# Kernel tuning notes

Hardware: AMD Instinct MI355X
Metric: run time of the kernel (lower is better)

The kernel has to match this reference:

```python
import jax, jax.numpy as jnp
import numpy as np

D_MODEL = 1024
N_HEADS = 16
HEAD_DIM = D_MODEL // N_HEADS  # 64
BASE = 10000.0
MAX_X, MAX_Y, MAX_Z = 32, 32, 8
NEG_INF = -1e9  # stand-in for float('-inf') in masked_fill; identical after softmax


def _split_dims(head_dim):
    n_pairs = head_dim // 2
    px = n_pairs // 3
    py = n_pairs // 3
    pz = n_pairs - px - py
    return px * 2, py * 2, pz * 2


def _cos_sin_table(dim, max_pos):
    # matches RotaryEmbedding3D._register_cache
    inv_freq = 1.0 / (BASE ** (np.arange(0, dim, 2, dtype=np.float32) / dim))
    t = np.arange(max_pos, dtype=np.float32)[:, None] * inv_freq  # [max_pos, dim/2]
    cos = np.repeat(np.cos(t), 2, axis=-1)  # repeat_interleave(2)
    sin = np.repeat(np.sin(t), 2, axis=-1)
    return jnp.asarray(cos), jnp.asarray(sin)


def _rotate_half(x):
    x1 = x[..., ::2]
    x2 = x[..., 1::2]
    return jnp.stack((-x2, x1), axis=-1).reshape(x.shape)


def setup_inputs() -> dict:
    key = jax.random.key(0)
    k1, k2, k3, k4, k5, k6 = jax.random.split(key, 6)
    B, S = 2, 2048
    hidden_states = jax.random.normal(k1, (B, S, D_MODEL), dtype=jnp.float32)
    w_qkv = jax.random.normal(k2, (D_MODEL, 3 * D_MODEL), dtype=jnp.float32) * 0.02
    w_out = jax.random.normal(k3, (D_MODEL, D_MODEL), dtype=jnp.float32) * 0.02
    px = jax.random.randint(k4, (B, S, 1), 0, MAX_X)
    py = jax.random.randint(k5, (B, S, 1), 0, MAX_Y)
    pz = jax.random.randint(k6, (B, S, 1), 0, MAX_Z)
    pos_xyz = jnp.concatenate([px, py, pz], axis=-1).astype(jnp.int64)
    causal_mask = jnp.triu(jnp.ones((S, S), dtype=bool), k=1)[None, None]  # [1,1,S,S]
    return {"hidden_states": hidden_states, "w_qkv": w_qkv, "w_out": w_out,
            "pos_xyz": pos_xyz, "causal_mask": causal_mask}


def reference(hidden_states, w_qkv, w_out, pos_xyz, causal_mask):
    B, S, D = hidden_states.shape
    H, Hd = N_HEADS, HEAD_DIM
    # fused QKV projection
    qkv = hidden_states @ w_qkv  # [B,S,3D]
    qkv = qkv.reshape(B, S, 3, H, Hd).transpose(2, 0, 3, 1, 4)  # [3,B,H,S,Hd]
    q, k, v = qkv[0], qkv[1], qkv[2]
    # 3D RoPE tables and lookups
    dx, dy, dz = _split_dims(Hd)
    cx, sx = _cos_sin_table(dx, MAX_X)
    cy, sy = _cos_sin_table(dy, MAX_Y)
    cz, sz = _cos_sin_table(dz, MAX_Z)
    ix = jnp.clip(pos_xyz[..., 0], 0, MAX_X - 1)
    iy = jnp.clip(pos_xyz[..., 1], 0, MAX_Y - 1)
    iz = jnp.clip(pos_xyz[..., 2], 0, MAX_Z - 1)
    cos = jnp.concatenate([cx[ix], cy[iy], cz[iz]], axis=-1)[:, None]  # [B,1,S,Hd]
    sin = jnp.concatenate([sx[ix], sy[iy], sz[iz]], axis=-1)[:, None]
    q = q * cos + _rotate_half(q) * sin
    k = k * cos + _rotate_half(k) * sin
    # SDPA with causal bias
    scale = Hd ** -0.5
    scores = jnp.einsum('bhqd,bhkd->bhqk', q, k) * scale
    scores = jnp.where(causal_mask, jnp.asarray(NEG_INF, scores.dtype), scores)
    probs = jax.nn.softmax(scores, axis=-1)
    attn = jnp.einsum('bhqk,bhkd->bhqd', probs, v)
    attn = attn.transpose(0, 2, 1, 3).reshape(B, S, D)
    return attn @ w_out
```

## Files before the change

kernel.cpp:

```cpp
#include <hip/hip_runtime.h>
#include <hip/hip_bf16.h>
#include <math.h>

typedef __bf16 bf16;
typedef __bf16 bf16x8 __attribute__((ext_vector_type(8)));
typedef float f32x4 __attribute__((ext_vector_type(4)));

#define SEQ 2048
#define NHEADS 16
#define HDIM 64
#define DM 1024
#define NEGBIG -1.0e30f

__device__ __forceinline__ void gload_lds16(const void* g, void* l) {
  __builtin_amdgcn_global_load_lds(
      (const __attribute__((address_space(1))) unsigned int*)g,
      (__attribute__((address_space(3))) unsigned int*)l, 16, 0, 0);
}

template <int CTRL>
__device__ __forceinline__ float dppmovf(float x) {
  return __builtin_bit_cast(
      float, __builtin_amdgcn_mov_dpp(__builtin_bit_cast(int, x), CTRL, 0xf,
                                      0xf, true));
}
__device__ __forceinline__ float rowmax16(float x) {
  x = fmaxf(x, dppmovf<0xB1>(x));
  x = fmaxf(x, dppmovf<0x4E>(x));
  x = fmaxf(x, dppmovf<0x124>(x));
  x = fmaxf(x, dppmovf<0x128>(x));
  return x;
}
__device__ __forceinline__ float rowsum16(float x) {
  x += dppmovf<0xB1>(x);
  x += dppmovf<0x4E>(x);
  x += dppmovf<0x124>(x);
  x += dppmovf<0x128>(x);
  return x;
}

__global__ __launch_bounds__(256) void cvt_f32_bf16(
    const float* __restrict__ in, bf16* __restrict__ out) {
  int i = (blockIdx.x * 256 + threadIdx.x) * 8;
  float4 a = *(const float4*)(in + i);
  float4 b = *(const float4*)(in + i + 4);
  bf16x8 o;
  o[0] = (bf16)a.x; o[1] = (bf16)a.y; o[2] = (bf16)a.z; o[3] = (bf16)a.w;
  o[4] = (bf16)b.x; o[5] = (bf16)b.y; o[6] = (bf16)b.z; o[7] = (bf16)b.w;
  *(bf16x8*)(out + i) = o;
}

__global__ __launch_bounds__(256) void transpose_f32_bf16(
    const float* __restrict__ in, bf16* __restrict__ out, int R, int C) {
  __shared__ float tile[64][65];
  int t = threadIdx.x;
  int c0 = blockIdx.x * 64, r0 = blockIdx.y * 64;
  int col = t & 63, rb = (t >> 6) * 16;
#pragma unroll
  for (int i = 0; i < 16; ++i)
    tile[rb + i][col] = in[(size_t)(r0 + rb + i) * C + c0 + col];
  __syncthreads();
#pragma unroll
  for (int i = 0; i < 16; ++i)
    out[(size_t)(c0 + rb + i) * R + r0 + col] = (bf16)tile[col][rb + i];
}

template <int EPI>
__global__ __launch_bounds__(256) void gemm_bt(
    const bf16* __restrict__ A, const bf16* __restrict__ Bt,
    float* __restrict__ C, int M, int N, int K,
    bf16* __restrict__ q_ws, bf16* __restrict__ k_ws, bf16* __restrict__ vT_ws,
    const int* __restrict__ pos) {
  __shared__ __align__(16) bf16 a_lds[128 * 32];
  __shared__ __align__(16) bf16 b_lds[128 * 32];
  int tid = threadIdx.x;
  int wave = tid >> 6, lane = tid & 63;
  int quad = lane >> 4, l15 = lane & 15;
  int wm = wave >> 1, wn = wave & 1;
  int m0 = blockIdx.y * 128, n0 = blockIdx.x * 128;

  f32x4 acc[4][4] = {};

  for (int kt = 0; kt < K; kt += 32) {
    __syncthreads();
#pragma unroll
    for (int call = 0; call < 2; ++call) {
      int chunk = call * 256 + tid;
      int row = chunk >> 2, cc = (chunk & 3) * 8;
      gload_lds16(A + (size_t)(m0 + row) * K + kt + cc,
                  (char*)a_lds + call * 4096 + wave * 1024);
      gload_lds16(Bt + (size_t)(n0 + row) * K + kt + cc,
                  (char*)b_lds + call * 4096 + wave * 1024);
    }
    __syncthreads();
    bf16x8 af[4], bfr[4];
#pragma unroll
    for (int i = 0; i < 4; ++i) {
      af[i]  = *(const bf16x8*)(a_lds + (wm * 64 + i * 16 + l15) * 32 + quad * 8);
      bfr[i] = *(const bf16x8*)(b_lds + (wn * 64 + i * 16 + l15) * 32 + quad * 8);
    }
#pragma unroll
    for (int mi = 0; mi < 4; ++mi)
#pragma unroll
      for (int ni = 0; ni < 4; ++ni)
        acc[mi][ni] = __builtin_amdgcn_mfma_f32_16x16x32_bf16(
            af[mi], bfr[ni], acc[mi][ni], 0, 0, 0);
  }

  if (EPI == 0) {
#pragma unroll
    for (int mi = 0; mi < 4; ++mi) {
      int mb = m0 + wm * 64 + mi * 16 + quad * 4;
#pragma unroll
      for (int ni = 0; ni < 4; ++ni) {
        int n = n0 + wn * 64 + ni * 16 + l15;
#pragma unroll
        for (int r = 0; r < 4; ++r)
          C[(size_t)(mb + r) * N + n] = acc[mi][ni][r];
      }
    }
  } else {
    const float LN1E4 = 9.210340371976184f;
#pragma unroll
    for (int mi = 0; mi < 4; ++mi) {
#pragma unroll
      for (int r = 0; r < 4; ++r) {
        int m = m0 + wm * 64 + mi * 16 + quad * 4 + r;
        int b = m >> 11, s = m & 2047;
        int px = pos[m * 3 + 0], py = pos[m * 3 + 1], pz = pos[m * 3 + 2];
        px = px < 0 ? 0 : (px > 31 ? 31 : px);
        py = py < 0 ? 0 : (py > 31 ? 31 : py);
        pz = pz < 0 ? 0 : (pz > 7 ? 7 : pz);
#pragma unroll
        for (int ni = 0; ni < 4; ++ni) {
          int n = n0 + wn * 64 + ni * 16 + l15;
          float v = acc[mi][ni][r];
          float partner = __shfl_xor(v, 1, 64);
          int which = n >> 10, nn = n & 1023, h = nn >> 6, hd = nn & 63;
          if (which == 2) {
            vT_ws[((size_t)(b * NHEADS + h) * HDIM + hd) * SEQ + s] = (bf16)v;
          } else {
            int i = hd >> 1, p, d, iloc;
            if (hd < 20)      { p = px; d = 20; iloc = i; }
            else if (hd < 40) { p = py; d = 20; iloc = i - 10; }
            else              { p = pz; d = 24; iloc = i - 20; }
            float invf = __expf(-((float)(2 * iloc) / (float)d) * LN1E4);
            float ang = (float)p * invf;
            float sn, cs;
            __sincosf(ang, &sn, &cs);
            float outv =
                (hd & 1) ? (v * cs + partner * sn) : (v * cs - partner * sn);
            bf16* dst = (which == 0) ? q_ws : k_ws;
            dst[((size_t)(b * NHEADS + h) * SEQ + s) * HDIM + hd] = (bf16)outv;
          }
        }
      }
    }
  }
}

__global__ __launch_bounds__(256) void attn_fwd(
    const bf16* __restrict__ Q, const bf16* __restrict__ K,
    const bf16* __restrict__ VT, bf16* __restrict__ O) {
  __shared__ __align__(16) bf16 k_lds[64 * 72];
  __shared__ __align__(16) bf16 v_lds[64 * 72];
  __shared__ __align__(16) bf16 p_lds[64 * 72];
  int tid = threadIdx.x;
  int wave = tid >> 6, lane = tid & 63;
  int quad = lane >> 4, l15 = lane & 15;
  int idx = blockIdx.x;
  int bh = idx & 31;
  int qt = 31 - (idx >> 5);
  int q0 = qt * 64;
  size_t base = (size_t)bh * SEQ * HDIM;
  const bf16* Qb = Q + base;
  const bf16* Kb = K + base;
  const bf16* VTb = VT + base;
  bf16* pw = p_lds + wave * 16 * 72;

  bf16x8 qf0 = *(const bf16x8*)(Qb + (size_t)(q0 + wave * 16 + l15) * HDIM + quad * 8);
  bf16x8 qf1 = *(const bf16x8*)(Qb + (size_t)(q0 + wave * 16 + l15) * HDIM + 32 + quad * 8);

  int c0 = tid * 2;
  int srow = c0 >> 3;
  int soff = (c0 & 7) * 8;

  f32x4 o_acc[4] = {};
  float m_i[4], l_i[4];
#pragma unroll
  for (int r = 0; r < 4; ++r) { m_i[r] = NEGBIG; l_i[r] = 0.f; }
  int qrow[4];
#pragma unroll
  for (int r = 0; r < 4; ++r) qrow[r] = q0 + wave * 16 + quad * 4 + r;

  for (int tkv = 0; tkv <= qt; ++tkv) {
    int kv0 = tkv * 64;
    __syncthreads();
    {
      const bf16* ksrc = Kb + (size_t)(kv0 + srow) * HDIM + soff;
      const bf16* vsrc = VTb + (size_t)srow * SEQ + kv0 + soff;
      bf16x8 ka = *(const bf16x8*)ksrc, kb2 = *(const bf16x8*)(ksrc + 8);
      bf16x8 va = *(const bf16x8*)vsrc, vb2 = *(const bf16x8*)(vsrc + 8);
      *(bf16x8*)(k_lds + srow * 72 + soff) = ka;
      *(bf16x8*)(k_lds + srow * 72 + soff + 8) = kb2;
      *(bf16x8*)(v_lds + srow * 72 + soff) = va;
      *(bf16x8*)(v_lds + srow * 72 + soff + 8) = vb2;
    }
    __syncthreads();
    f32x4 s_acc[4];
#pragma unroll
    for (int nt = 0; nt < 4; ++nt) {
      const bf16* krow_p = k_lds + (nt * 16 + l15) * 72;
      bf16x8 kf0 = *(const bf16x8*)(krow_p + quad * 8);
      bf16x8 kf1 = *(const bf16x8*)(krow_p + 32 + quad * 8);
      f32x4 z = {};
      z = __builtin_amdgcn_mfma_f32_16x16x32_bf16(qf0, kf0, z, 0, 0, 0);
      z = __builtin_amdgcn_mfma_f32_16x16x32_bf16(qf1, kf1, z, 0, 0, 0);
      s_acc[nt] = z;
    }
    bool diag = (tkv == qt);
#pragma unroll
    for (int r = 0; r < 4; ++r) {
      float mx = NEGBIG;
#pragma unroll
      for (int nt = 0; nt < 4; ++nt) {
        float v = fminf(s_acc[nt][r] * 0.125f, 3.0e38f);
        if (diag && (kv0 + nt * 16 + l15 > qrow[r])) v = NEGBIG;
        s_acc[nt][r] = v;
        mx = fmaxf(mx, v);
      }
      mx = rowmax16(mx);
      float mnew = fmaxf(m_i[r], mx);
      float alpha = __expf(m_i[r] - mnew);
      float rs = 0.f;
#pragma unroll
      for (int nt = 0; nt < 4; ++nt) {
        float p = __expf(s_acc[nt][r] - mnew);
        s_acc[nt][r] = p;
        rs += p;
      }
      rs = rowsum16(rs);
      l_i[r] = l_i[r] * alpha + rs;
      m_i[r] = mnew;
#pragma unroll
      for (int nt = 0; nt < 4; ++nt) o_acc[nt][r] *= alpha;
#pragma unroll
      for (int nt = 0; nt < 4; ++nt)
        pw[(quad * 4 + r) * 72 + nt * 16 + l15] = (bf16)s_acc[nt][r];
    }
    __asm__ volatile("s_waitcnt lgkmcnt(0)" ::: "memory");
    bf16x8 pf0 = *(const bf16x8*)(pw + l15 * 72 + quad * 8);
    bf16x8 pf1 = *(const bf16x8*)(pw + l15 * 72 + 32 + quad * 8);
#pragma unroll
    for (int nt = 0; nt < 4; ++nt) {
      const bf16* vrow = v_lds + (nt * 16 + l15) * 72;
      bf16x8 vf0 = *(const bf16x8*)(vrow + quad * 8);
      bf16x8 vf1 = *(const bf16x8*)(vrow + 32 + quad * 8);
      o_acc[nt] = __builtin_amdgcn_mfma_f32_16x16x32_bf16(pf0, vf0, o_acc[nt], 0, 0, 0);
      o_acc[nt] = __builtin_amdgcn_mfma_f32_16x16x32_bf16(pf1, vf1, o_acc[nt], 0, 0, 0);
    }
  }
  int b = bh >> 4, h = bh & 15;
#pragma unroll
  for (int r = 0; r < 4; ++r) {
    float inv = 1.f / l_i[r];
    int s = q0 + wave * 16 + quad * 4 + r;
#pragma unroll
    for (int nt = 0; nt < 4; ++nt) {
      int d = nt * 16 + l15;
      O[((size_t)(b * SEQ + s)) * DM + h * HDIM + d] = (bf16)(o_acc[nt][r] * inv);
    }
  }
}

extern "C" void kernel_launch(void* const* d_in, const int* in_sizes, int n_in,
                              void* d_out, int out_size, void* d_ws,
                              size_t ws_size, hipStream_t stream) {
  const float* hidden = (const float*)d_in[0];
  const float* w_qkv  = (const float*)d_in[1];
  const float* w_out  = (const float*)d_in[2];
  const int*   pos    = (const int*)d_in[3];
  float* out = (float*)d_out;

  char* ws = (char*)d_ws;
  bf16* wqkvT  = (bf16*)ws;  ws += (size_t)3072 * 1024 * 2;
  bf16* woutT  = (bf16*)ws;  ws += (size_t)1024 * 1024 * 2;
  bf16* hid_bf = (bf16*)ws;  ws += (size_t)4096 * 1024 * 2;
  bf16* q_ws   = (bf16*)ws;  ws += (size_t)32 * SEQ * HDIM * 2;
  bf16* k_ws   = (bf16*)ws;  ws += (size_t)32 * SEQ * HDIM * 2;
  bf16* vT_ws  = (bf16*)ws;  ws += (size_t)32 * SEQ * HDIM * 2;
  bf16* attn_ws = (bf16*)ws;

  cvt_f32_bf16<<<dim3(2048), 256, 0, stream>>>(hidden, hid_bf);
  transpose_f32_bf16<<<dim3(48, 16), 256, 0, stream>>>(w_qkv, wqkvT, 1024, 3072);
  transpose_f32_bf16<<<dim3(16, 16), 256, 0, stream>>>(w_out, woutT, 1024, 1024);
  gemm_bt<1><<<dim3(24, 32), 256, 0, stream>>>(
      hid_bf, wqkvT, nullptr, 4096, 3072, 1024, q_ws, k_ws, vT_ws, pos);
  attn_fwd<<<dim3(1024), 256, 0, stream>>>(q_ws, k_ws, vT_ws, attn_ws);
  gemm_bt<0><<<dim3(8, 32), 256, 0, stream>>>(
      attn_ws, woutT, out, 4096, 1024, 1024, nullptr, nullptr, nullptr, nullptr);
}
```

Before: 227.8 us.

## Precompute RoPE table in LDS, remap GEMM tiles per XCD, tweak attention masking

Result: slower. 238.5 us (+4.7%).

```diff
diff --git a/kernel.cpp b/kernel.cpp
--- a/kernel.cpp
+++ b/kernel.cpp
@@ -73,11 +73,32 @@
     const int* __restrict__ pos) {
   __shared__ __align__(16) bf16 a_lds[128 * 32];
   __shared__ __align__(16) bf16 b_lds[128 * 32];
+  __shared__ float2 rope_tbl[EPI == 1 ? 32 * 64 : 1];
   int tid = threadIdx.x;
   int wave = tid >> 6, lane = tid & 63;
   int quad = lane >> 4, l15 = lane & 15;
   int wm = wave >> 1, wn = wave & 1;
-  int m0 = blockIdx.y * 128, n0 = blockIdx.x * 128;
+
+  int flat = blockIdx.y * gridDim.x + blockIdx.x;
+  int mband = gridDim.y >> 3;
+  int xcd = flat & 7, sidx = flat >> 3;
+  int m0 = (xcd * mband + (sidx % mband)) * 128;
+  int n0 = (sidx / mband) * 128;
+
+  if (EPI == 1) {
+    const float LN1E4 = 9.210340371976184f;
+    for (int e = tid; e < 2048; e += 256) {
+      int p = e >> 6, hd = e & 63;
+      int i = hd >> 1, d, iloc;
+      if (hd < 20)      { d = 20; iloc = i; }
+      else if (hd < 40) { d = 20; iloc = i - 10; }
+      else              { d = 24; iloc = i - 20; }
+      float invf = __expf(-((float)(2 * iloc) / (float)d) * LN1E4);
+      float sn, cs;
+      __sincosf((float)p * invf, &sn, &cs);
+      rope_tbl[e] = make_float2(cs, (hd & 1) ? sn : -sn);
+    }
+  }
 
   f32x4 acc[4][4] = {};
 
@@ -120,7 +141,6 @@
       }
     }
   } else {
-    const float LN1E4 = 9.210340371976184f;
 #pragma unroll
     for (int mi = 0; mi < 4; ++mi) {
 #pragma unroll
@@ -140,16 +160,9 @@
           if (which == 2) {
             vT_ws[((size_t)(b * NHEADS + h) * HDIM + hd) * SEQ + s] = (bf16)v;
           } else {
-            int i = hd >> 1, p, d, iloc;
-            if (hd < 20)      { p = px; d = 20; iloc = i; }
-            else if (hd < 40) { p = py; d = 20; iloc = i - 10; }
-            else              { p = pz; d = 24; iloc = i - 20; }
-            float invf = __expf(-((float)(2 * iloc) / (float)d) * LN1E4);
-            float ang = (float)p * invf;
-            float sn, cs;
-            __sincosf(ang, &sn, &cs);
-            float outv =
-                (hd & 1) ? (v * cs + partner * sn) : (v * cs - partner * sn);
+            int p = hd < 20 ? px : (hd < 40 ? py : pz);
+            float2 cs = rope_tbl[p * 64 + hd];
+            float outv = v * cs.x + partner * cs.y;
             bf16* dst = (which == 0) ? q_ws : k_ws;
             dst[((size_t)(b * NHEADS + h) * SEQ + s) * HDIM + hd] = (bf16)outv;
           }
@@ -164,7 +177,7 @@
     const bf16* __restrict__ VT, bf16* __restrict__ O) {
   __shared__ __align__(16) bf16 k_lds[64 * 72];
   __shared__ __align__(16) bf16 v_lds[64 * 72];
-  __shared__ __align__(16) bf16 p_lds[64 * 72];
+  __shared__ __align__(16) bf16 p_lds[64 * 80];
   int tid = threadIdx.x;
   int wave = tid >> 6, lane = tid & 63;
   int quad = lane >> 4, l15 = lane & 15;
@@ -176,7 +189,7 @@
   const bf16* Qb = Q + base;
   const bf16* Kb = K + base;
   const bf16* VTb = VT + base;
-  bf16* pw = p_lds + wave * 16 * 72;
+  bf16* pw = p_lds + wave * 16 * 80;
 
   bf16x8 qf0 = *(const bf16x8*)(Qb + (size_t)(q0 + wave * 16 + l15) * HDIM + quad * 8);
   bf16x8 qf1 = *(const bf16x8*)(Qb + (size_t)(q0 + wave * 16 + l15) * HDIM + 32 + quad * 8);
@@ -218,14 +231,19 @@
       z = __builtin_amdgcn_mfma_f32_16x16x32_bf16(qf1, kf1, z, 0, 0, 0);
       s_acc[nt] = z;
     }
-    bool diag = (tkv == qt);
+    if (tkv == qt) {
+#pragma unroll
+      for (int r = 0; r < 4; ++r)
+#pragma unroll
+        for (int nt = 0; nt < 4; ++nt)
+          if (kv0 + nt * 16 + l15 > qrow[r]) s_acc[nt][r] = NEGBIG * 8.f;
+    }
 #pragma unroll
     for (int r = 0; r < 4; ++r) {
       float mx = NEGBIG;
 #pragma unroll
       for (int nt = 0; nt < 4; ++nt) {
-        float v = fminf(s_acc[nt][r] * 0.125f, 3.0e38f);
-        if (diag && (kv0 + nt * 16 + l15 > qrow[r])) v = NEGBIG;
+        float v = s_acc[nt][r] * 0.125f;
         s_acc[nt][r] = v;
         mx = fmaxf(mx, v);
       }
@@ -246,11 +264,11 @@
       for (int nt = 0; nt < 4; ++nt) o_acc[nt][r] *= alpha;
 #pragma unroll
       for (int nt = 0; nt < 4; ++nt)
-        pw[(quad * 4 + r) * 72 + nt * 16 + l15] = (bf16)s_acc[nt][r];
+        pw[(quad * 4 + r) * 80 + nt * 16 + l15] = (bf16)s_acc[nt][r];
     }
     __asm__ volatile("s_waitcnt lgkmcnt(0)" ::: "memory");
-    bf16x8 pf0 = *(const bf16x8*)(pw + l15 * 72 + quad * 8);
-    bf16x8 pf1 = *(const bf16x8*)(pw + l15 * 72 + 32 + quad * 8);
+    bf16x8 pf0 = *(const bf16x8*)(pw + l15 * 80 + quad * 8);
+    bf16x8 pf1 = *(const bf16x8*)(pw + l15 * 80 + 32 + quad * 8);
 #pragma unroll
     for (int nt = 0; nt < 4; ++nt) {
       const bf16* vrow = v_lds + (nt * 16 + l15) * 72;
```
